# Performance work log

Measured on AMD Instinct MI355X. Metric: run time of the kernel, lower is better.

The kernel has to match this reference:

```python
import jax, jax.numpy as jnp
import numpy as np

KERNEL = 3
STRIDE = 1
PAD = 1


def setup_inputs() -> dict:
    key = jax.random.key(0)
    k1, k2 = jax.random.split(key)
    x = jax.random.normal(k1, (16, 32, 512, 512), dtype=jnp.float32)
    # original init: torch.rand(O, I, k, k) / (k*k)
    kernels = jax.random.uniform(k2, (32, 32, KERNEL, KERNEL), dtype=jnp.float32) / (KERNEL * KERNEL)
    return {"x": x, "kernels": kernels}


def reference(x, kernels):
    # Equivalent math to the unfold+einsum im2col conv2d: pad, extract kxk
    # windows with stride, contract over (in_channels, kh, kw).
    # Expressed as a direct convolution (cross-correlation), which is the
    # same computation without materializing the 6D window tensor.
    out = jax.lax.conv_general_dilated(
        x, kernels,
        window_strides=(STRIDE, STRIDE),
        padding=((PAD, PAD), (PAD, PAD)),
        dimension_numbers=("NCHW", "OIHW", "NCHW"),
    )
    return out  # [B, out_channels, H_out, W_out]
```

## Files before the change

### kernel.cpp

```cpp
#include <hip/hip_runtime.h>
#include <hip/hip_bf16.h>

typedef __attribute__((ext_vector_type(8))) short bf16x8;
typedef __attribute__((ext_vector_type(4))) float f32x4;
typedef __attribute__((ext_vector_type(4))) unsigned int u32x4;

#define HH 512
#define WWD 512
#define HW (HH * WWD)
#define TW 64
#define SLOTS 6
#define PXG (SLOTS * 66)
#define XBYTES (4 * PXG * 16)
#define WOFF XBYTES
#define DUMMY (WOFF + 18432)
#define NITER 32

__device__ __forceinline__ unsigned short f2bf(float f) {
    unsigned u = __builtin_bit_cast(unsigned, f);
    u += 0x7FFFu + ((u >> 16) & 1u);
    return (unsigned short)(u >> 16);
}

__device__ __forceinline__ void issue2(const float* __restrict__ xb, int row0, int w0,
                                       float (&sv)[3][8]) {
    #pragma unroll
    for (int k = 0; k < 3; ++k) {
        if (k == 2 && threadIdx.x >= 32) continue;
        int u = (k < 2) ? (int)threadIdx.x + k * 256 : 512 + (int)threadIdx.x;
        int g = u / 136, r = u - g * 136, hh = r / 68, ww = r - hh * 68;
        int wwc = ww < 66 ? ww : 65;
        int row = row0 + hh, cl = w0 + wwc - 1;
        bool ok = (ww < 66) & ((unsigned)row < 512u) & ((unsigned)cl < 512u);
        int rowc = row < 0 ? 0 : (row > 511 ? 511 : row);
        int clc  = cl  < 0 ? 0 : (cl  > 511 ? 511 : cl);
        const float* src = xb + (size_t)(g * 8) * HW + rowc * WWD + clc;
        #pragma unroll
        for (int j = 0; j < 8; ++j) { float v = src[(size_t)j * HW]; sv[k][j] = ok ? v : 0.f; }
    }
}

__device__ __forceinline__ void write2(char* smem, int wsb, float (&sv)[3][8]) {
    #pragma unroll
    for (int k = 0; k < 3; ++k) {
        if (k == 2 && threadIdx.x >= 32) continue;
        int u = (k < 2) ? (int)threadIdx.x + k * 256 : 512 + (int)threadIdx.x;
        int g = u / 136, r = u - g * 136, hh = r / 68, ww = r - hh * 68;
        int slot = wsb + hh; if (slot >= SLOTS) slot -= SLOTS;
        int byte = (ww < 66) ? (g * PXG + slot * 66 + ww) * 16
                             : (DUMMY + (threadIdx.x & 63) * 16);
        unsigned q0 = (unsigned)f2bf(sv[k][0]) | ((unsigned)f2bf(sv[k][1]) << 16);
        unsigned q1 = (unsigned)f2bf(sv[k][2]) | ((unsigned)f2bf(sv[k][3]) << 16);
        unsigned q2 = (unsigned)f2bf(sv[k][4]) | ((unsigned)f2bf(sv[k][5]) << 16);
        unsigned q3 = (unsigned)f2bf(sv[k][6]) | ((unsigned)f2bf(sv[k][7]) << 16);
        u32x4 q = { q0, q1, q2, q3 };
        *(u32x4*)(smem + byte) = q;
    }
}

template<bool WR, bool ISS, bool BAR>
__device__ __forceinline__ void conv_body(char* smem, const float* __restrict__ xb,
                                          float* __restrict__ ob,
                                          float (&cur)[3][8], float (&nxt)[3][8],
                                          int srb, int rowbase, int issrow, int w0,
                                          int wv, int col16, int g4) {
    if (WR) {
        asm volatile("s_waitcnt vmcnt(4)" ::: "memory");
        __builtin_amdgcn_sched_barrier(0);
        int wsb = srb + 4; if (wsb >= SLOTS) wsb -= SLOTS;
        write2(smem, wsb, cur);
    }
    if (ISS) issue2(xb, issrow, w0, nxt);

    f32x4 acc[2][2];
    {
        f32x4 z = {0.f, 0.f, 0.f, 0.f};
        acc[0][0] = z; acc[0][1] = z; acc[1][0] = z; acc[1][1] = z;
    }
    int rs[3];
    #pragma unroll
    for (int dh = 0; dh < 3; ++dh) {
        int s = srb + (wv & 1) + dh; if (s >= SLOTS) s -= SLOTS;
        rs[dh] = s * 66;
    }
    const int wcb = (wv >> 1) * 32;
    const char* xg = smem + g4 * (PXG * 16);
    const char* wg = smem + WOFF + g4 * 512 + col16 * 16;
    #pragma unroll
    for (int dh = 0; dh < 3; ++dh) {
        #pragma unroll
        for (int dw = 0; dw < 3; ++dw) {
            const int tap = dh * 3 + dw;
            bf16x8 b0 = *(const bf16x8*)(wg + tap * 2048);
            bf16x8 b1 = *(const bf16x8*)(wg + tap * 2048 + 256);
            #pragma unroll
            for (int m = 0; m < 2; ++m) {
                bf16x8 a = *(const bf16x8*)(xg + (rs[dh] + wcb + m * 16 + col16 + dw) * 16);
                acc[m][0] = __builtin_amdgcn_mfma_f32_16x16x32_bf16(a, b0, acc[m][0], 0, 0, 0);
                acc[m][1] = __builtin_amdgcn_mfma_f32_16x16x32_bf16(a, b1, acc[m][1], 0, 0, 0);
            }
        }
    }
    {
        float* orow = ob + (size_t)(rowbase + (wv & 1)) * WWD + w0 + wcb;
        #pragma unroll
        for (int m = 0; m < 2; ++m)
            #pragma unroll
            for (int n = 0; n < 2; ++n)
                *(f32x4*)(orow + (size_t)(n * 16 + col16) * HW + m * 16 + g4 * 4) = acc[m][n];
    }
    if (BAR) {
        asm volatile("s_waitcnt lgkmcnt(0)" ::: "memory");
        __builtin_amdgcn_sched_barrier(0);
        __builtin_amdgcn_s_barrier();
        __builtin_amdgcn_sched_barrier(0);
    }
}

__global__ __launch_bounds__(256, 3)
void conv3x3_mfma(const float* __restrict__ x,
                  const float* __restrict__ wk,
                  float* __restrict__ out) {
    __shared__ __align__(16) char smem[DUMMY + 1024];

    const int tid   = threadIdx.x;
    const int lane  = tid & 63;
    const int wv    = tid >> 6;
    const int col16 = lane & 15;
    const int g4    = lane >> 4;

    const int w0    = blockIdx.x * TW;
    const int hbase = blockIdx.y * (2 * NITER);
    const int b     = blockIdx.z;

    const float* xb = x + (size_t)b * 32 * HW;
    float* ob = out + (size_t)b * 32 * HW;

    {
        unsigned short* wl = (unsigned short*)(smem + WOFF);
        for (int i = tid; i < 9216; i += 256) {
            int oc = i / 288; int rem = i - oc * 288;
            int ic = rem / 9; int tap = rem - ic * 9;
            wl[((tap * 4 + (ic >> 3)) * 32 + oc) * 8 + (ic & 7)] = f2bf(wk[i]);
        }
    }

    {
        float svp[5][8];
        #pragma unroll
        for (int k = 0; k < 5; ++k) {
            if (k == 4 && tid >= 32) continue;
            int u = (k < 4) ? tid + k * 256 : 1024 + tid;
            int g = u / 264, p = u - g * 264, hh = p / 66, ww = p - hh * 66;
            int row = hbase + hh - 1, cl = w0 + ww - 1;
            bool ok = ((unsigned)row < 512u) & ((unsigned)cl < 512u);
            int rowc = row < 0 ? 0 : (row > 511 ? 511 : row);
            int clc  = cl  < 0 ? 0 : (cl  > 511 ? 511 : cl);
            const float* src = xb + (size_t)(g * 8) * HW + rowc * WWD + clc;
            #pragma unroll
            for (int j = 0; j < 8; ++j) { float v = src[(size_t)j * HW]; svp[k][j] = ok ? v : 0.f; }
        }
        #pragma unroll
        for (int k = 0; k < 5; ++k) {
            if (k == 4 && tid >= 32) continue;
            int u = (k < 4) ? tid + k * 256 : 1024 + tid;
            int g = u / 264, p = u - g * 264;
            unsigned q0 = (unsigned)f2bf(svp[k][0]) | ((unsigned)f2bf(svp[k][1]) << 16);
            unsigned q1 = (unsigned)f2bf(svp[k][2]) | ((unsigned)f2bf(svp[k][3]) << 16);
            unsigned q2 = (unsigned)f2bf(svp[k][4]) | ((unsigned)f2bf(svp[k][5]) << 16);
            unsigned q3 = (unsigned)f2bf(svp[k][6]) | ((unsigned)f2bf(svp[k][7]) << 16);
            u32x4 q = { q0, q1, q2, q3 };
            *(u32x4*)(smem + (g * PXG + p) * 16) = q;
        }
    }

    float svA[3][8], svB[3][8];
    issue2(xb, hbase + 3, w0, svA);
    __builtin_amdgcn_sched_barrier(0);
    __syncthreads();

    int srb = 0;
    conv_body<1, 1, 1>(smem, xb, ob, svA, svB, 0, hbase, hbase + 5, w0, wv, col16, g4);
    srb = 2;
    #pragma unroll 1
    for (int tp = 0; tp < 14; ++tp) {
        int t1 = 1 + 2 * tp;
        conv_body<1, 1, 1>(smem, xb, ob, svB, svA, srb,
                           hbase + 2 * t1, hbase + 2 * t1 + 5, w0, wv, col16, g4);
        srb += 2; if (srb >= SLOTS) srb -= SLOTS;
        conv_body<1, 1, 1>(smem, xb, ob, svA, svB, srb,
                           hbase + 2 * (t1 + 1), hbase + 2 * (t1 + 1) + 5, w0, wv, col16, g4);
        srb += 2; if (srb >= SLOTS) srb -= SLOTS;
    }
    conv_body<1, 1, 1>(smem, xb, ob, svB, svA, srb, hbase + 58, hbase + 63, w0, wv, col16, g4);
    srb += 2; if (srb >= SLOTS) srb -= SLOTS;
    conv_body<1, 0, 1>(smem, xb, ob, svA, svB, srb, hbase + 60, 0, w0, wv, col16, g4);
    srb += 2; if (srb >= SLOTS) srb -= SLOTS;
    conv_body<0, 0, 0>(smem, xb, ob, svB, svA, srb, hbase + 62, 0, w0, wv, col16, g4);
}

extern "C" void kernel_launch(void* const* d_in, const int* in_sizes, int n_in,
                              void* d_out, int out_size, void* d_ws, size_t ws_size,
                              hipStream_t stream) {
    const float* x  = (const float*)d_in[0];
    const float* wk = (const float*)d_in[1];
    float* out = (float*)d_out;
    dim3 grid(WWD / TW, HH / (2 * NITER), 16);
    conv3x3_mfma<<<grid, 256, 0, stream>>>(x, wk, out);
}
```

Baseline: 286.8 us.

## Stage input rows via global_load_lds double buffer and keep weights in registers

Replaces the register-staged prefetch of the next input rows with direct global-to-LDS async loads into a double-buffered fp32 staging area, then converts from staging to the bf16 tile in LDS each step. Weight fragments are converted once and held in registers for all taps instead of being re-read from LDS per tap. The goal is to cut register pressure from the prefetch buffers and hide global latency better. In exchange it uses more LDS, drops occupancy from 3 to 2 blocks per CU, and adds an extra LDS read/write pass per step.

```diff
diff --git a/kernel.cpp b/kernel.cpp
--- a/kernel.cpp
+++ b/kernel.cpp
@@ -5,16 +5,17 @@
 typedef __attribute__((ext_vector_type(4))) float f32x4;
 typedef __attribute__((ext_vector_type(4))) unsigned int u32x4;
 
-#define HH 512
-#define WWD 512
-#define HW (HH * WWD)
+#define HW (512 * 512)
 #define TW 64
 #define SLOTS 6
 #define PXG (SLOTS * 66)
-#define XBYTES (4 * PXG * 16)
-#define WOFF XBYTES
-#define DUMMY (WOFF + 18432)
+#define TILE_B (4 * PXG * 16)
+#define STAGE_HALF 20480
+#define SREAL 18432
+#define DUMMY (TILE_B + 2 * STAGE_HALF)
 #define NITER 32
+
+#define SCHED() __builtin_amdgcn_sched_barrier(0)
 
 __device__ __forceinline__ unsigned short f2bf(float f) {
     unsigned u = __builtin_bit_cast(unsigned, f);
@@ -22,55 +23,65 @@
     return (unsigned short)(u >> 16);
 }
 
-__device__ __forceinline__ void issue2(const float* __restrict__ xb, int row0, int w0,
-                                       float (&sv)[3][8]) {
-    #pragma unroll
-    for (int k = 0; k < 3; ++k) {
-        if (k == 2 && threadIdx.x >= 32) continue;
-        int u = (k < 2) ? (int)threadIdx.x + k * 256 : 512 + (int)threadIdx.x;
-        int g = u / 136, r = u - g * 136, hh = r / 68, ww = r - hh * 68;
-        int wwc = ww < 66 ? ww : 65;
-        int row = row0 + hh, cl = w0 + wwc - 1;
-        bool ok = (ww < 66) & ((unsigned)row < 512u) & ((unsigned)cl < 512u);
-        int rowc = row < 0 ? 0 : (row > 511 ? 511 : row);
-        int clc  = cl  < 0 ? 0 : (cl  > 511 ? 511 : cl);
-        const float* src = xb + (size_t)(g * 8) * HW + rowc * WWD + clc;
-        #pragma unroll
-        for (int j = 0; j < 8; ++j) { float v = src[(size_t)j * HW]; sv[k][j] = ok ? v : 0.f; }
-    }
-}
-
-__device__ __forceinline__ void write2(char* smem, int wsb, float (&sv)[3][8]) {
-    #pragma unroll
-    for (int k = 0; k < 3; ++k) {
-        if (k == 2 && threadIdx.x >= 32) continue;
-        int u = (k < 2) ? (int)threadIdx.x + k * 256 : 512 + (int)threadIdx.x;
-        int g = u / 136, r = u - g * 136, hh = r / 68, ww = r - hh * 68;
-        int slot = wsb + hh; if (slot >= SLOTS) slot -= SLOTS;
-        int byte = (ww < 66) ? (g * PXG + slot * 66 + ww) * 16
-                             : (DUMMY + (threadIdx.x & 63) * 16);
-        unsigned q0 = (unsigned)f2bf(sv[k][0]) | ((unsigned)f2bf(sv[k][1]) << 16);
-        unsigned q1 = (unsigned)f2bf(sv[k][2]) | ((unsigned)f2bf(sv[k][3]) << 16);
-        unsigned q2 = (unsigned)f2bf(sv[k][4]) | ((unsigned)f2bf(sv[k][5]) << 16);
-        unsigned q3 = (unsigned)f2bf(sv[k][6]) | ((unsigned)f2bf(sv[k][7]) << 16);
-        u32x4 q = { q0, q1, q2, q3 };
-        *(u32x4*)(smem + byte) = q;
-    }
-}
-
-template<bool WR, bool ISS, bool BAR>
-__device__ __forceinline__ void conv_body(char* smem, const float* __restrict__ xb,
-                                          float* __restrict__ ob,
-                                          float (&cur)[3][8], float (&nxt)[3][8],
-                                          int srb, int rowbase, int issrow, int w0,
-                                          int wv, int col16, int g4) {
-    if (WR) {
-        asm volatile("s_waitcnt vmcnt(4)" ::: "memory");
-        __builtin_amdgcn_sched_barrier(0);
-        int wsb = srb + 4; if (wsb >= SLOTS) wsb -= SLOTS;
-        write2(smem, wsb, cur);
-    }
-    if (ISS) issue2(xb, issrow, w0, nxt);
+__device__ __forceinline__ void gll16(const float* g, char* l) {
+    __builtin_amdgcn_global_load_lds(
+        (const __attribute__((address_space(1))) void*)g,
+        (__attribute__((address_space(3))) void*)l, 16, 0, 0);
+}
+
+__device__ __forceinline__ void issue_stage(const float* __restrict__ xb, int row0,
+                                            int w0, char* smem, int half, int wvu) {
+    const int lane = (int)threadIdx.x & 63;
+    char* base = smem + TILE_B + half * STAGE_HALF;
+    #pragma unroll
+    for (int i = 0; i < 5; ++i) {
+        int ob = (wvu * 5 + i) * 1024;
+        int o  = ob + lane * 16;
+        int o2 = o < (SREAL - 1) ? o : (SREAL - 1);
+        int ch = o2 / 576;
+        int rem = o2 - ch * 576;
+        int hh = rem / 288;
+        int wl = (rem - hh * 288) >> 2;
+        int row = row0 + hh; row = row < 511 ? row : 511;
+        int cb = w0 - 4 + wl;
+        cb = cb < 0 ? 0 : (cb > 508 ? 508 : cb);
+        gll16(xb + (size_t)ch * HW + row * 512 + cb, base + ob);
+    }
+}
+
+template<bool TRANS, bool GLL, bool BAR>
+__device__ __forceinline__ void body(char* smem, const float* __restrict__ xb,
+                                     float* __restrict__ ob, bf16x8 (&wf)[9][2],
+                                     int srb, int half, int rowbase, int w0,
+                                     int wv, int wvu, int col16, int g4) {
+    if (GLL) issue_stage(xb, rowbase + 5, w0, smem, half ^ 1, wvu);
+
+    if (TRANS) {
+        const char* sb = smem + TILE_B + half * STAGE_HALF;
+        const int rowA = rowbase + 3;
+        #pragma unroll
+        for (int k = 0; k < 3; ++k) {
+            if (k == 2 && threadIdx.x >= 32) continue;
+            int u = (k < 2) ? (int)threadIdx.x + k * 256 : 512 + (int)threadIdx.x;
+            int g = u / 136, r = u - g * 136, sl = r / 68, ww = r - sl * 68;
+            float v[8];
+            int ba = g * 8 * 576 + sl * 288 + (ww + 3) * 4;
+            #pragma unroll
+            for (int j = 0; j < 8; ++j) v[j] = *(const float*)(sb + ba + j * 576);
+            bool ok = (ww < 66) & ((unsigned)(w0 + ww - 1) < 512u) & (rowA + sl < 512);
+            #pragma unroll
+            for (int j = 0; j < 8; ++j) v[j] = ok ? v[j] : 0.f;
+            unsigned q0 = (unsigned)f2bf(v[0]) | ((unsigned)f2bf(v[1]) << 16);
+            unsigned q1 = (unsigned)f2bf(v[2]) | ((unsigned)f2bf(v[3]) << 16);
+            unsigned q2 = (unsigned)f2bf(v[4]) | ((unsigned)f2bf(v[5]) << 16);
+            unsigned q3 = (unsigned)f2bf(v[6]) | ((unsigned)f2bf(v[7]) << 16);
+            int slot = srb + 4 + sl; if (slot >= SLOTS) slot -= SLOTS;
+            int byte = (ww < 66) ? (g * PXG + slot * 66 + ww) * 16
+                                 : (DUMMY + ((int)threadIdx.x & 63) * 16);
+            u32x4 q = { q0, q1, q2, q3 };
+            *(u32x4*)(smem + byte) = q;
+        }
+    }
 
     f32x4 acc[2][2];
     {
@@ -85,118 +96,122 @@
     }
     const int wcb = (wv >> 1) * 32;
     const char* xg = smem + g4 * (PXG * 16);
-    const char* wg = smem + WOFF + g4 * 512 + col16 * 16;
     #pragma unroll
     for (int dh = 0; dh < 3; ++dh) {
         #pragma unroll
         for (int dw = 0; dw < 3; ++dw) {
             const int tap = dh * 3 + dw;
-            bf16x8 b0 = *(const bf16x8*)(wg + tap * 2048);
-            bf16x8 b1 = *(const bf16x8*)(wg + tap * 2048 + 256);
             #pragma unroll
             for (int m = 0; m < 2; ++m) {
                 bf16x8 a = *(const bf16x8*)(xg + (rs[dh] + wcb + m * 16 + col16 + dw) * 16);
-                acc[m][0] = __builtin_amdgcn_mfma_f32_16x16x32_bf16(a, b0, acc[m][0], 0, 0, 0);
-                acc[m][1] = __builtin_amdgcn_mfma_f32_16x16x32_bf16(a, b1, acc[m][1], 0, 0, 0);
+                acc[m][0] = __builtin_amdgcn_mfma_f32_16x16x32_bf16(a, wf[tap][0], acc[m][0], 0, 0, 0);
+                acc[m][1] = __builtin_amdgcn_mfma_f32_16x16x32_bf16(a, wf[tap][1], acc[m][1], 0, 0, 0);
             }
         }
     }
     {
-        float* orow = ob + (size_t)(rowbase + (wv & 1)) * WWD + w0 + wcb;
+        float* orow = ob + (size_t)(rowbase + (wv & 1)) * 512 + w0 + wcb;
         #pragma unroll
         for (int m = 0; m < 2; ++m)
             #pragma unroll
             for (int n = 0; n < 2; ++n)
                 *(f32x4*)(orow + (size_t)(n * 16 + col16) * HW + m * 16 + g4 * 4) = acc[m][n];
     }
+
     if (BAR) {
+        asm volatile("s_waitcnt vmcnt(4)" ::: "memory");
+        SCHED();
         asm volatile("s_waitcnt lgkmcnt(0)" ::: "memory");
-        __builtin_amdgcn_sched_barrier(0);
+        SCHED();
         __builtin_amdgcn_s_barrier();
-        __builtin_amdgcn_sched_barrier(0);
-    }
-}
-
-__global__ __launch_bounds__(256, 3)
+        SCHED();
+    }
+}
+
+__global__ __launch_bounds__(256, 2)
 void conv3x3_mfma(const float* __restrict__ x,
                   const float* __restrict__ wk,
                   float* __restrict__ out) {
     __shared__ __align__(16) char smem[DUMMY + 1024];
 
-    const int tid   = threadIdx.x;
+    const int tid   = (int)threadIdx.x;
     const int lane  = tid & 63;
     const int wv    = tid >> 6;
+    const int wvu   = __builtin_amdgcn_readfirstlane(wv);
     const int col16 = lane & 15;
     const int g4    = lane >> 4;
 
     const int w0    = blockIdx.x * TW;
-    const int hbase = blockIdx.y * (2 * NITER);
+    const int hbase = blockIdx.y * 64;
     const int b     = blockIdx.z;
 
     const float* xb = x + (size_t)b * 32 * HW;
     float* ob = out + (size_t)b * 32 * HW;
 
     {
-        unsigned short* wl = (unsigned short*)(smem + WOFF);
+        float* ws = (float*)(smem + TILE_B);
         for (int i = tid; i < 9216; i += 256) {
-            int oc = i / 288; int rem = i - oc * 288;
-            int ic = rem / 9; int tap = rem - ic * 9;
-            wl[((tap * 4 + (ic >> 3)) * 32 + oc) * 8 + (ic & 7)] = f2bf(wk[i]);
-        }
-    }
-
-    {
-        float svp[5][8];
-        #pragma unroll
-        for (int k = 0; k < 5; ++k) {
-            if (k == 4 && tid >= 32) continue;
-            int u = (k < 4) ? tid + k * 256 : 1024 + tid;
-            int g = u / 264, p = u - g * 264, hh = p / 66, ww = p - hh * 66;
-            int row = hbase + hh - 1, cl = w0 + ww - 1;
-            bool ok = ((unsigned)row < 512u) & ((unsigned)cl < 512u);
-            int rowc = row < 0 ? 0 : (row > 511 ? 511 : row);
-            int clc  = cl  < 0 ? 0 : (cl  > 511 ? 511 : cl);
-            const float* src = xb + (size_t)(g * 8) * HW + rowc * WWD + clc;
-            #pragma unroll
-            for (int j = 0; j < 8; ++j) { float v = src[(size_t)j * HW]; svp[k][j] = ok ? v : 0.f; }
-        }
-        #pragma unroll
-        for (int k = 0; k < 5; ++k) {
-            if (k == 4 && tid >= 32) continue;
-            int u = (k < 4) ? tid + k * 256 : 1024 + tid;
-            int g = u / 264, p = u - g * 264;
-            unsigned q0 = (unsigned)f2bf(svp[k][0]) | ((unsigned)f2bf(svp[k][1]) << 16);
-            unsigned q1 = (unsigned)f2bf(svp[k][2]) | ((unsigned)f2bf(svp[k][3]) << 16);
-            unsigned q2 = (unsigned)f2bf(svp[k][4]) | ((unsigned)f2bf(svp[k][5]) << 16);
-            unsigned q3 = (unsigned)f2bf(svp[k][6]) | ((unsigned)f2bf(svp[k][7]) << 16);
-            u32x4 q = { q0, q1, q2, q3 };
-            *(u32x4*)(smem + (g * PXG + p) * 16) = q;
-        }
-    }
-
-    float svA[3][8], svB[3][8];
-    issue2(xb, hbase + 3, w0, svA);
-    __builtin_amdgcn_sched_barrier(0);
+            int oc = i / 288;
+            ws[oc * 289 + (i - oc * 288)] = wk[i];
+        }
+    }
+    float svp[5][8];
+    #pragma unroll
+    for (int k = 0; k < 5; ++k) {
+        if (k == 4 && tid >= 32) continue;
+        int u = (k < 4) ? tid + k * 256 : 1024 + tid;
+        int g = u / 264, p = u - g * 264, hh = p / 66, ww = p - hh * 66;
+        int row = hbase + hh - 1, cl = w0 + ww - 1;
+        bool ok = ((unsigned)row < 512u) & ((unsigned)cl < 512u);
+        int rowc = row < 0 ? 0 : (row > 511 ? 511 : row);
+        int clc  = cl  < 0 ? 0 : (cl  > 511 ? 511 : cl);
+        const float* src = xb + (size_t)(g * 8) * HW + rowc * 512 + clc;
+        #pragma unroll
+        for (int j = 0; j < 8; ++j) { float v = src[(size_t)j * HW]; svp[k][j] = ok ? v : 0.f; }
+    }
     __syncthreads();
 
+    bf16x8 wf[9][2];
+    {
+        const float* ws = (const float*)(smem + TILE_B);
+        #pragma unroll
+        for (int tap = 0; tap < 9; ++tap) {
+            #pragma unroll
+            for (int n = 0; n < 2; ++n) {
+                bf16x8 f;
+                #pragma unroll
+                for (int j = 0; j < 8; ++j)
+                    f[j] = (short)f2bf(ws[(n * 16 + col16) * 289 + (g4 * 8 + j) * 9 + tap]);
+                wf[tap][n] = f;
+            }
+        }
+    }
+    __syncthreads();
+
+    #pragma unroll
+    for (int k = 0; k < 5; ++k) {
+        if (k == 4 && tid >= 32) continue;
+        int u = (k < 4) ? tid + k * 256 : 1024 + tid;
+        int g = u / 264, p = u - g * 264;
+        unsigned q0 = (unsigned)f2bf(svp[k][0]) | ((unsigned)f2bf(svp[k][1]) << 16);
+        unsigned q1 = (unsigned)f2bf(svp[k][2]) | ((unsigned)f2bf(svp[k][3]) << 16);
+        unsigned q2 = (unsigned)f2bf(svp[k][4]) | ((unsigned)f2bf(svp[k][5]) << 16);
+        unsigned q3 = (unsigned)f2bf(svp[k][6]) | ((unsigned)f2bf(svp[k][7]) << 16);
+        u32x4 q = { q0, q1, q2, q3 };
+        *(u32x4*)(smem + (g * PXG + p) * 16) = q;
+    }
+    issue_stage(xb, hbase + 3, w0, smem, 0, wvu);
+    __syncthreads();
+
     int srb = 0;
-    conv_body<1, 1, 1>(smem, xb, ob, svA, svB, 0, hbase, hbase + 5, w0, wv, col16, g4);
-    srb = 2;
     #pragma unroll 1
-    for (int tp = 0; tp < 14; ++tp) {
-        int t1 = 1 + 2 * tp;
-        conv_body<1, 1, 1>(smem, xb, ob, svB, svA, srb,
-                           hbase + 2 * t1, hbase + 2 * t1 + 5, w0, wv, col16, g4);
+    for (int t = 0; t < 30; ++t) {
+        body<1, 1, 1>(smem, xb, ob, wf, srb, t & 1, hbase + 2 * t, w0, wv, wvu, col16, g4);
         srb += 2; if (srb >= SLOTS) srb -= SLOTS;
-        conv_body<1, 1, 1>(smem, xb, ob, svA, svB, srb,
-                           hbase + 2 * (t1 + 1), hbase + 2 * (t1 + 1) + 5, w0, wv, col16, g4);
-        srb += 2; if (srb >= SLOTS) srb -= SLOTS;
-    }
-    conv_body<1, 1, 1>(smem, xb, ob, svB, svA, srb, hbase + 58, hbase + 63, w0, wv, col16, g4);
+    }
+    body<1, 0, 1>(smem, xb, ob, wf, srb, 0, hbase + 60, w0, wv, wvu, col16, g4);
     srb += 2; if (srb >= SLOTS) srb -= SLOTS;
-    conv_body<1, 0, 1>(smem, xb, ob, svA, svB, srb, hbase + 60, 0, w0, wv, col16, g4);
-    srb += 2; if (srb >= SLOTS) srb -= SLOTS;
-    conv_body<0, 0, 0>(smem, xb, ob, svB, svA, srb, hbase + 62, 0, w0, wv, col16, g4);
+    body<0, 0, 0>(smem, xb, ob, wf, srb, 1, hbase + 62, w0, wv, wvu, col16, g4);
 }
 
 extern "C" void kernel_launch(void* const* d_in, const int* in_sizes, int n_in,
@@ -205,6 +220,6 @@
     const float* x  = (const float*)d_in[0];
     const float* wk = (const float*)d_in[1];
     float* out = (float*)d_out;
-    dim3 grid(WWD / TW, HH / (2 * NITER), 16);
+    dim3 grid(512 / TW, 512 / 64, 16);
     conv3x3_mfma<<<grid, 256, 0, stream>>>(x, wk, out);
 }
```

Result: faster. 273.5 us (-4.6%).
